# Kernel tuning notes

Measured on AMD Instinct MI355X. Metric: run time of the kernel, lower is better.

Reference implementation:

```python
import jax, jax.numpy as jnp
import numpy as np

N_HEAD = 16
N_BLOCKS = 2
EPS = 1e-6

def _rmsnorm(x, g):
    return x * jax.lax.rsqrt(jnp.mean(x * x, axis=-1, keepdims=True) + EPS) * g

def _causal_sa(x, Wqkv, Wproj, g):
    # x: (B, T, C); fused qkv, RMSNorm on q/k over full C before head split
    B, T, C = x.shape
    hd = C // N_HEAD
    q, k, v = jnp.split(x @ Wqkv, 3, axis=-1)
    q = _rmsnorm(q, g)
    k = _rmsnorm(k, g)
    def heads(t):
        return t.reshape(B, T, N_HEAD, hd).transpose(0, 2, 1, 3)
    q, k, v = heads(q), heads(k), heads(v)
    scores = jnp.einsum('bhqd,bhkd->bhqk', q, k) * (1.0 / np.sqrt(hd))
    mask = jnp.tril(jnp.ones((T, T), dtype=bool))
    scores = jnp.where(mask, scores, -jnp.finfo(scores.dtype).max)
    att = jax.nn.softmax(scores, axis=-1)
    y = jnp.einsum('bhqk,bhkd->bhqd', att, v)
    y = y.transpose(0, 2, 1, 3).reshape(B, T, C)
    return y @ Wproj

def setup_inputs() -> dict:
    key = jax.random.key(0)
    ks = jax.random.split(key, 8)
    B, ng, T, C = 2, 8, 256, 1024
    M_loc, M_glob = 16, 16
    s = 0.02
    return {
        'x': jax.random.normal(ks[0], (B, ng, T, C), jnp.float32),
        'mem_tokens': jax.random.normal(ks[1], (B, M_glob, C), jnp.float32),
        'local_mem': jax.random.normal(ks[2], (B, ng, M_loc, C), jnp.float32),
        'Wqkv_loc': jax.random.normal(ks[3], (N_BLOCKS, C, 3 * C), jnp.float32) * s,
        'Wproj_loc': jax.random.normal(ks[4], (N_BLOCKS, C, C), jnp.float32) * s,
        'g_loc': jnp.ones((N_BLOCKS, C), jnp.float32),
        'Wqkv_glob': jax.random.normal(ks[5], (N_BLOCKS, C, 3 * C), jnp.float32) * s,
        'Wproj_glob': jax.random.normal(ks[6], (N_BLOCKS, C, C), jnp.float32) * s,
        'g_glob': jnp.ones((N_BLOCKS, C), jnp.float32),
    }

def reference(x, mem_tokens, local_mem, Wqkv_loc, Wproj_loc, g_loc, Wqkv_glob, Wproj_glob, g_glob):
    B, ng, T, C = x.shape
    M_loc = local_mem.shape[2]
    M_glob = mem_tokens.shape[1]
    for i in range(N_BLOCKS):
        # local causal SA: per-group, with local mem tokens prepended
        xl = jnp.concatenate([local_mem, x], axis=2).reshape(B * ng, M_loc + T, C)
        yl = _causal_sa(xl, Wqkv_loc[i], Wproj_loc[i], g_loc[i])
        yl = yl.reshape(B, ng, M_loc + T, C)
        local_mem = yl[:, :, :M_loc, :]
        x = yl[:, :, M_loc:, :]
        # global causal SA over flattened sequence with global mem tokens
        xg = x.reshape(B, ng * T, C)
        xg = jnp.concatenate([mem_tokens, xg], axis=1)
        yg = _causal_sa(xg, Wqkv_glob[i], Wproj_glob[i], g_glob[i])
        mem_tokens = yg[:, :M_glob, :]
        x = yg[:, M_glob:, :].reshape(B, ng, T, C)
    return x
```

## Files before the change

### kernel.cpp

```cpp
#include <hip/hip_runtime.h>
#include <hip/hip_bf16.h>
#include <math.h>

typedef __attribute__((ext_vector_type(8))) short s16x8;
typedef __attribute__((ext_vector_type(4))) short s16x4;
typedef __attribute__((ext_vector_type(4))) float f32x4;

#define MPAD 4352
#define LG 2064
#define CT 8
#define SM_SHIFT 11.5415603f

__device__ __forceinline__ short f2b(float f) {
  unsigned u = __float_as_uint(f);
  unsigned r = (u + 0x7fffu + ((u >> 16) & 1u)) >> 16;
  return (short)(unsigned short)r;
}
__device__ __forceinline__ float b2f(short s) {
  return __uint_as_float(((unsigned)(unsigned short)s) << 16);
}
__device__ __forceinline__ float fexp2(float x) {
#if __has_builtin(__builtin_amdgcn_exp2f)
  return __builtin_amdgcn_exp2f(x);
#else
  float r;
  asm("v_exp_f32 %0, %1" : "=v"(r) : "v"(x));
  return r;
#endif
}
__device__ __forceinline__ int cvtpk(float lo, float hi) {
  int r;
  asm("v_cvt_pk_bf16_f32 %0, %1, %2" : "=v"(r) : "v"(lo), "v"(hi));
  return r;
}

__device__ __forceinline__ void gl_lds16(const short* g, short* l) {
  __builtin_amdgcn_global_load_lds((const __attribute__((address_space(1))) short*)g,
                                   (__attribute__((address_space(3))) short*)l, 16, 0, 0);
}

__global__ __launch_bounds__(256) void transpose_cast(const float* __restrict__ in,
                                                      short* __restrict__ out,
                                                      int K, int N) {
  __shared__ float tile[32][33];
  int bn = blockIdx.x * 32;
  int bk = blockIdx.y * 32;
  for (int i = threadIdx.y; i < 32; i += 8)
    tile[i][threadIdx.x] = in[(size_t)(bk + i) * N + bn + threadIdx.x];
  __syncthreads();
  for (int i = threadIdx.y; i < 32; i += 8)
    out[(size_t)(bn + i) * K + bk + threadIdx.x] = f2b(tile[threadIdx.x][i]);
}

__global__ __launch_bounds__(256) void transpose_v(const short* __restrict__ QKV,
                                                   short* __restrict__ Vt,
                                                   int L, int Lpad) {
  __shared__ short tile[32][33];
  int sh = blockIdx.z;
  int s = sh >> 4, h = sh & 15;
  int kb = blockIdx.x * 32;
  int cb = blockIdx.y * 32;
  int tx = threadIdx.x;
  for (int i = threadIdx.y; i < 32; i += 8) {
    int key = kb + i;
    if (key > L - 1) key = L - 1;
    tile[i][tx] = QKV[(size_t)(s * L + key) * 3072 + 2048 + h * 64 + cb + tx];
  }
  __syncthreads();
  for (int i = threadIdx.y; i < 32; i += 8)
    Vt[((size_t)sh * 64 + cb + i) * Lpad + kb + tx] = tile[tx][i];
}

#define QROW(MI, AX)                                                                  \
  acc[MI][0] = __builtin_amdgcn_mfma_f32_16x16x32_bf16(AX, b0, acc[MI][0], 0, 0, 0);  \
  acc[MI][1] = __builtin_amdgcn_mfma_f32_16x16x32_bf16(AX, b1, acc[MI][1], 0, 0, 0);  \
  acc[MI][2] = __builtin_amdgcn_mfma_f32_16x16x32_bf16(AX, b2, acc[MI][2], 0, 0, 0);  \
  acc[MI][3] = __builtin_amdgcn_mfma_f32_16x16x32_bf16(AX, b3, acc[MI][3], 0, 0, 0);

#define RD12(B, S)                                                              \
  a0 = rdA(B, S, 0); a1 = rdA(B, S, 1); a2 = rdA(B, S, 2); a3 = rdA(B, S, 3);   \
  a4 = rdA(B, S, 4); a5 = rdA(B, S, 5); a6 = rdA(B, S, 6); a7 = rdA(B, S, 7);   \
  b0 = rdB(B, S, 0); b1 = rdB(B, S, 1); b2 = rdB(B, S, 2); b3 = rdB(B, S, 3);

__global__ __launch_bounds__(512, 2) void gemm_8ph(const short* __restrict__ A,
                                                   const short* __restrict__ BT,
                                                   short* __restrict__ C,
                                                   int K, int N) {
  extern __shared__ short lds[];
  short* Asb = lds;
  short* Bsb = lds + 32768;
  const int tid = threadIdx.x;
  const int lane = tid & 63, wid = tid >> 6;
  const int wm = wid >> 2, wn = wid & 3;
  const int l15 = lane & 15, lhi = lane >> 4;
  const int m0 = blockIdx.y * 256;
  const int n0 = blockIdx.x * 256;

  f32x4 acc[8][4] = {};

  auto stageA = [&](int b, int h, int kt) {
#pragma unroll
    for (int j = 0; j < 2; ++j) {
      int u = j * 512 + tid;
      int row = u >> 3, slot = u & 7;
      int ss = slot ^ (row & 7);
      gl_lds16(A + (size_t)(m0 + h * 128 + row) * K + kt * 64 + ss * 8,
               Asb + (b * 2 + h) * 8192 + u * 8);
    }
  };
  auto stageB = [&](int b, int h, int kt) {
#pragma unroll
    for (int j = 0; j < 2; ++j) {
      int u = j * 512 + tid;
      int row = u >> 3, slot = u & 7;
      int ss = slot ^ (row & 7);
      gl_lds16(BT + (size_t)(n0 + h * 128 + row) * K + kt * 64 + ss * 8,
               Bsb + (b * 2 + h) * 8192 + u * 8);
    }
  };
  auto rdA = [&](int b, int s, int mf) -> s16x8 {
    int row = mf * 16 + l15;
    int sl = ((s << 2) | lhi) ^ (row & 7);
    return *(const s16x8*)(Asb + (b * 2 + wm) * 8192 + row * 64 + sl * 8);
  };
  auto rdB = [&](int b, int s, int nf) -> s16x8 {
    int row = (wn & 1) * 64 + nf * 16 + l15;
    int sl = ((s << 2) | lhi) ^ (row & 7);
    return *(const s16x8*)(Bsb + (b * 2 + (wn >> 1)) * 8192 + row * 64 + sl * 8);
  };

  const int NT = K >> 7;

  stageA(0, 0, 0); stageA(0, 1, 0); stageB(0, 0, 0); stageB(0, 1, 0);
  stageA(1, 0, 1); stageA(1, 1, 1);
  asm volatile("s_waitcnt vmcnt(4)" ::: "memory");
  __builtin_amdgcn_s_barrier();

  s16x8 a0, a1, a2, a3, a4, a5, a6, a7, b0, b1, b2, b3;

  for (int t = 0; t < NT; ++t) {
    const bool last = (t == NT - 1);
    const int kt1 = 2 * t + 1;
    RD12(0, 0)
    stageB(1, 0, kt1);
    __builtin_amdgcn_s_barrier();
    __builtin_amdgcn_s_setprio(1);
    QROW(0, a0) QROW(1, a1) QROW(2, a2) QROW(3, a3)
    __builtin_amdgcn_s_setprio(0);
    __builtin_amdgcn_s_barrier();
    stageB(1, 1, kt1);
    __builtin_amdgcn_s_barrier();
    __builtin_amdgcn_s_setprio(1);
    QROW(4, a4) QROW(5, a5) QROW(6, a6) QROW(7, a7)
    __builtin_amdgcn_s_setprio(0);
    __builtin_amdgcn_s_barrier();
    RD12(0, 1)
    __builtin_amdgcn_s_barrier();
    __builtin_amdgcn_s_setprio(1);
    QROW(0, a0) QROW(1, a1) QROW(2, a2) QROW(3, a3)
    __builtin_amdgcn_s_setprio(0);
    __builtin_amdgcn_s_barrier();
    if (!last) {
      stageA(0, 0, 2 * t + 2); stageA(0, 1, 2 * t + 2);
      asm volatile("s_waitcnt vmcnt(4)" ::: "memory");
    } else {
      asm volatile("s_waitcnt vmcnt(0)" ::: "memory");
    }
    __builtin_amdgcn_s_barrier();
    __builtin_amdgcn_s_setprio(1);
    QROW(4, a4) QROW(5, a5) QROW(6, a6) QROW(7, a7)
    __builtin_amdgcn_s_setprio(0);
    __builtin_amdgcn_s_barrier();
    RD12(1, 0)
    if (!last) stageB(0, 0, 2 * t + 2);
    __builtin_amdgcn_s_barrier();
    __builtin_amdgcn_s_setprio(1);
    QROW(0, a0) QROW(1, a1) QROW(2, a2) QROW(3, a3)
    __builtin_amdgcn_s_setprio(0);
    __builtin_amdgcn_s_barrier();
    if (!last) stageB(0, 1, 2 * t + 2);
    __builtin_amdgcn_s_barrier();
    __builtin_amdgcn_s_setprio(1);
    QROW(4, a4) QROW(5, a5) QROW(6, a6) QROW(7, a7)
    __builtin_amdgcn_s_setprio(0);
    __builtin_amdgcn_s_barrier();
    RD12(1, 1)
    __builtin_amdgcn_s_barrier();
    __builtin_amdgcn_s_setprio(1);
    QROW(0, a0) QROW(1, a1) QROW(2, a2) QROW(3, a3)
    __builtin_amdgcn_s_setprio(0);
    __builtin_amdgcn_s_barrier();
    if (!last) {
      stageA(1, 0, kt1 + 2); stageA(1, 1, kt1 + 2);
      asm volatile("s_waitcnt vmcnt(4)" ::: "memory");
    }
    __builtin_amdgcn_s_barrier();
    __builtin_amdgcn_s_setprio(1);
    QROW(4, a4) QROW(5, a5) QROW(6, a6) QROW(7, a7)
    __builtin_amdgcn_s_setprio(0);
    __builtin_amdgcn_s_barrier();
  }

#pragma unroll
  for (int mf = 0; mf < 8; ++mf) {
    int row_base = m0 + wm * 128 + mf * 16 + lhi * 4;
#pragma unroll
    for (int nf = 0; nf < 4; ++nf) {
      int col = n0 + wn * 64 + nf * 16 + l15;
#pragma unroll
      for (int r = 0; r < 4; ++r)
        C[(size_t)(row_base + r) * N + col] = f2b(acc[mf][nf][r]);
    }
  }
}

__global__ __launch_bounds__(256) void gemm_bt3(const short* __restrict__ A,
                                                const short* __restrict__ BT,
                                                short* __restrict__ C,
                                                int K, int N) {
  __shared__ short As[2][128 * 32];
  __shared__ short Bs[2][128 * 32];
  const int tid = threadIdx.x;
  const int lane = tid & 63;
  const int w = tid >> 6;
  const int wr = (w >> 1) * 64, wc = (w & 1) * 64;
  const int m0 = blockIdx.y * 128;
  const int n0 = blockIdx.x * 128;
  const int l15 = lane & 15, lhi = lane >> 4;

  f32x4 acc[4][4] = {};

  auto STAGE = [&](int b, int k0) {
#pragma unroll
    for (int p = 0; p < 2; ++p) {
      int g = w * 128 + p * 64 + lane;
      int row = g >> 2;
      int cs = (g & 3) * 8;
      gl_lds16(A + (size_t)(m0 + row) * K + k0 + cs, &As[b][g * 8]);
      gl_lds16(BT + (size_t)(n0 + row) * K + k0 + cs, &Bs[b][g * 8]);
    }
  };

  const int nt = K >> 5;
  STAGE(0, 0);
  __syncthreads();
  int cur = 0;
  for (int t = 0; t < nt; ++t) {
    if (t + 1 < nt) STAGE(cur ^ 1, (t + 1) << 5);
    s16x8 af[4], bf[4];
#pragma unroll
    for (int m = 0; m < 4; ++m)
      af[m] = *(const s16x8*)(&As[cur][(wr + m * 16 + l15) * 32 + lhi * 8]);
#pragma unroll
    for (int n = 0; n < 4; ++n)
      bf[n] = *(const s16x8*)(&Bs[cur][(wc + n * 16 + l15) * 32 + lhi * 8]);
#pragma unroll
    for (int m = 0; m < 4; ++m)
#pragma unroll
      for (int n = 0; n < 4; ++n)
        acc[m][n] = __builtin_amdgcn_mfma_f32_16x16x32_bf16(af[m], bf[n], acc[m][n], 0, 0, 0);
    __syncthreads();
    cur ^= 1;
  }
#pragma unroll
  for (int m = 0; m < 4; ++m) {
    int row_base = m0 + wr + m * 16 + lhi * 4;
#pragma unroll
    for (int n = 0; n < 4; ++n) {
      int col = n0 + wc + n * 16 + l15;
#pragma unroll
      for (int r = 0; r < 4; ++r)
        C[(size_t)(row_base + r) * N + col] = f2b(acc[m][n][r]);
    }
  }
}

__global__ __launch_bounds__(256) void rmsnorm_qk(short* __restrict__ QKV,
                                                  const float* __restrict__ g) {
  int row = blockIdx.x;
  int which = blockIdx.y;
  size_t base = (size_t)row * 3072 + (size_t)which * 1024;
  int t = threadIdx.x;
  s16x4 in = *(const s16x4*)(QKV + base + t * 4);
  float v[4];
  float ss = 0.f;
#pragma unroll
  for (int j = 0; j < 4; ++j) {
    v[j] = b2f(in[j]);
    ss += v[j] * v[j];
  }
#pragma unroll
  for (int m = 32; m >= 1; m >>= 1) ss += __shfl_xor(ss, m);
  __shared__ float red[4];
  if ((t & 63) == 0) red[t >> 6] = ss;
  __syncthreads();
  float tot = red[0] + red[1] + red[2] + red[3];
  float inv = rsqrtf(tot * (1.0f / 1024.0f) + 1e-6f);
  if (which == 0) inv *= 0.125f * 1.44269504f;
  s16x4 out;
#pragma unroll
  for (int j = 0; j < 4; ++j) out[j] = f2b(v[j] * inv * g[t * 4 + j]);
  *(s16x4*)(&QKV[base + t * 4]) = out;
}

__global__ __launch_bounds__(256) void attn_causal4(const short* __restrict__ QKV,
                                                    const short* __restrict__ Vt,
                                                    short* __restrict__ Y,
                                                    int L, int Lpad) {
  const int h = blockIdx.y, s = blockIdx.z;
  const int q0 = blockIdx.x * 64;
  const int tid = threadIdx.x;
  const int lane = tid & 63, w = tid >> 6;
  const int l15 = lane & 15, lhi = lane >> 4;
  const int row0 = s * L;

  __shared__ short Ks[2][64][72];
  __shared__ short Vs[2][64][72];

  int qld = q0 + w * 16 + l15;
  if (qld > L - 1) qld = L - 1;
  const size_t qrow = (size_t)(row0 + qld) * 3072 + h * 64;
  s16x8 qf0 = *(const s16x8*)(QKV + qrow + lhi * 8);
  s16x8 qf1 = *(const s16x8*)(QKV + qrow + 32 + lhi * 8);

  float lsum = 0.f;
  f32x4 o[4];
#pragma unroll
  for (int d = 0; d < 4; ++d) o[d] = f32x4{0.f, 0.f, 0.f, 0.f};

  const short* Vbase = Vt + (size_t)(s * 16 + h) * 64 * Lpad;
  const int sA = (lhi & 1) * 32 + l15;
  const int sB = sA + 16;
  const int bh = lhi >> 1;

  s16x8 kreg[2], vreg[2];
#pragma unroll
  for (int p = 0; p < 2; ++p) {
    int g = tid + p * 256;
    int kr = g >> 3, cs = (g & 7) * 8;
    int krow = kr;
    if (krow > L - 1) krow = L - 1;
    kreg[p] = *(const s16x8*)(QKV + (size_t)(row0 + krow) * 3072 + 1024 + h * 64 + cs);
    vreg[p] = *(const s16x8*)(Vbase + (size_t)kr * Lpad + cs);
  }

  int buf = 0;
  for (int kb = 0; kb <= q0; kb += 64, buf ^= 1) {
#pragma unroll
    for (int p = 0; p < 2; ++p) {
      int g = tid + p * 256;
      int kr = g >> 3, cs = (g & 7) * 8;
      *(s16x8*)(&Ks[buf][kr][cs]) = kreg[p];
      *(s16x8*)(&Vs[buf][kr][cs]) = vreg[p];
    }
    __syncthreads();
    if (kb + 64 <= q0) {
#pragma unroll
      for (int p = 0; p < 2; ++p) {
        int g = tid + p * 256;
        int kr = g >> 3, cs = (g & 7) * 8;
        int krow = kb + 64 + kr;
        if (krow > L - 1) krow = L - 1;
        kreg[p] = *(const s16x8*)(QKV + (size_t)(row0 + krow) * 3072 + 1024 + h * 64 + cs);
        vreg[p] = *(const s16x8*)(Vbase + (size_t)kr * Lpad + kb + 64 + cs);
      }
    }

    f32x4 st[4];
#pragma unroll
    for (int n = 0; n < 4; ++n) {
      s16x8 k0 = *(const s16x8*)(&Ks[buf][n * 16 + l15][lhi * 8]);
      s16x8 k1 = *(const s16x8*)(&Ks[buf][n * 16 + l15][32 + lhi * 8]);
      f32x4 sa = f32x4{-SM_SHIFT, -SM_SHIFT, -SM_SHIFT, -SM_SHIFT};
      sa = __builtin_amdgcn_mfma_f32_16x16x32_bf16(k0, qf0, sa, 0, 0, 0);
      sa = __builtin_amdgcn_mfma_f32_16x16x32_bf16(k1, qf1, sa, 0, 0, 0);
      st[n] = sa;
    }

    if (kb == q0) {
      int q = q0 + w * 16 + l15;
#pragma unroll
      for (int n = 0; n < 4; ++n) {
#pragma unroll
        for (int r = 0; r < 4; ++r) {
          int key = kb + n * 16 + lhi * 4 + r;
          if (key > q) st[n][r] = -1e30f;
        }
      }
    }

    int wd[4][2];
#pragma unroll
    for (int n = 0; n < 4; ++n) {
      float p0 = fexp2(st[n][0]), p1 = fexp2(st[n][1]);
      float p2 = fexp2(st[n][2]), p3 = fexp2(st[n][3]);
      lsum += (p0 + p1) + (p2 + p3);
      wd[n][0] = cvtpk(p0, p1);
      wd[n][1] = cvtpk(p2, p3);
    }

#pragma unroll
    for (int kk = 0; kk < 2; ++kk) {
      int a0 = __shfl(wd[2 * kk][0], sA), a1 = __shfl(wd[2 * kk][1], sA);
      int a2 = __shfl(wd[2 * kk][0], sB), a3 = __shfl(wd[2 * kk][1], sB);
      int c0 = __shfl(wd[2 * kk + 1][0], sA), c1 = __shfl(wd[2 * kk + 1][1], sA);
      int c2 = __shfl(wd[2 * kk + 1][0], sB), c3 = __shfl(wd[2 * kk + 1][1], sB);
      int pw[4];
      pw[0] = bh ? c0 : a0;
      pw[1] = bh ? c1 : a1;
      pw[2] = bh ? c2 : a2;
      pw[3] = bh ? c3 : a3;
      s16x8 pa = *(const s16x8*)pw;
#pragma unroll
      for (int d = 0; d < 4; ++d) {
        s16x8 vf = *(const s16x8*)(&Vs[buf][d * 16 + l15][kk * 32 + lhi * 8]);
        o[d] = __builtin_amdgcn_mfma_f32_16x16x32_bf16(pa, vf, o[d], 0, 0, 0);
      }
    }
  }

  lsum += __shfl_xor(lsum, 16);
  lsum += __shfl_xor(lsum, 32);
  float lsq[4];
#pragma unroll
  for (int r = 0; r < 4; ++r) lsq[r] = __shfl(lsum, lhi * 4 + r);
#pragma unroll
  for (int d = 0; d < 4; ++d) {
#pragma unroll
    for (int r = 0; r < 4; ++r) {
      int qr = q0 + w * 16 + lhi * 4 + r;
      if (qr < L)
        Y[(size_t)(row0 + qr) * 1024 + h * 64 + d * 16 + l15] = f2b(o[d][r] / lsq[r]);
    }
  }
}

__global__ __launch_bounds__(256) void attn_split2(const short* __restrict__ QKV,
                                                   const short* __restrict__ Vt,
                                                   float* __restrict__ o_acc,
                                                   float* __restrict__ ls_acc) {
  const int qb = blockIdx.x;
  const int chunk = blockIdx.y;
  const int sh = blockIdx.z;
  const int t0 = chunk * CT;
  if (t0 > qb) return;
  const int t1 = min(t0 + CT, qb + 1);
  const int h = sh & 15, s = sh >> 4;
  const int q0 = qb * 64;
  const int tid = threadIdx.x;
  const int lane = tid & 63, w = tid >> 6;
  const int l15 = lane & 15, lhi = lane >> 4;
  const int row0 = s * LG;
  const int Lpad = 2112;

  __shared__ short Ks[2][64][72];
  __shared__ short Vs[2][64][72];

  int qld = q0 + w * 16 + l15;
  if (qld > LG - 1) qld = LG - 1;
  const size_t qrow = (size_t)(row0 + qld) * 3072 + h * 64;
  s16x8 qf0 = *(const s16x8*)(QKV + qrow + lhi * 8);
  s16x8 qf1 = *(const s16x8*)(QKV + qrow + 32 + lhi * 8);

  float lsum = 0.f;
  f32x4 o[4];
#pragma unroll
  for (int d = 0; d < 4; ++d) o[d] = f32x4{0.f, 0.f, 0.f, 0.f};

  const short* Vbase = Vt + (size_t)sh * 64 * Lpad;
  const int sA = (lhi & 1) * 32 + l15;
  const int sB = sA + 16;
  const int bh = lhi >> 1;

  s16x8 kreg[2], vreg[2];
  const int kb0 = t0 * 64;
#pragma unroll
  for (int p = 0; p < 2; ++p) {
    int g = tid + p * 256;
    int kr = g >> 3, cs = (g & 7) * 8;
    int krow = kb0 + kr;
    if (krow > LG - 1) krow = LG - 1;
    kreg[p] = *(const s16x8*)(QKV + (size_t)(row0 + krow) * 3072 + 1024 + h * 64 + cs);
    vreg[p] = *(const s16x8*)(Vbase + (size_t)kr * Lpad + kb0 + cs);
  }

  int buf = 0;
  for (int t = t0; t < t1; ++t, buf ^= 1) {
    const int kb = t * 64;
#pragma unroll
    for (int p = 0; p < 2; ++p) {
      int g = tid + p * 256;
      int kr = g >> 3, cs = (g & 7) * 8;
      *(s16x8*)(&Ks[buf][kr][cs]) = kreg[p];
      *(s16x8*)(&Vs[buf][kr][cs]) = vreg[p];
    }
    __syncthreads();
    if (t + 1 < t1) {
#pragma unroll
      for (int p = 0; p < 2; ++p) {
        int g = tid + p * 256;
        int kr = g >> 3, cs = (g & 7) * 8;
        int krow = kb + 64 + kr;
        if (krow > LG - 1) krow = LG - 1;
        kreg[p] = *(const s16x8*)(QKV + (size_t)(row0 + krow) * 3072 + 1024 + h * 64 + cs);
        vreg[p] = *(const s16x8*)(Vbase + (size_t)kr * Lpad + kb + 64 + cs);
      }
    }

    f32x4 st[4];
#pragma unroll
    for (int n = 0; n < 4; ++n) {
      s16x8 k0 = *(const s16x8*)(&Ks[buf][n * 16 + l15][lhi * 8]);
      s16x8 k1 = *(const s16x8*)(&Ks[buf][n * 16 + l15][32 + lhi * 8]);
      f32x4 sa = f32x4{-SM_SHIFT, -SM_SHIFT, -SM_SHIFT, -SM_SHIFT};
      sa = __builtin_amdgcn_mfma_f32_16x16x32_bf16(k0, qf0, sa, 0, 0, 0);
      sa = __builtin_amdgcn_mfma_f32_16x16x32_bf16(k1, qf1, sa, 0, 0, 0);
      st[n] = sa;
    }

    if (t == qb) {
      int q = q0 + w * 16 + l15;
#pragma unroll
      for (int n = 0; n < 4; ++n) {
#pragma unroll
        for (int r = 0; r < 4; ++r) {
          int key = kb + n * 16 + lhi * 4 + r;
          if (key > q) st[n][r] = -1e30f;
        }
      }
    }

    int wd[4][2];
#pragma unroll
    for (int n = 0; n < 4; ++n) {
      float p0 = fexp2(st[n][0]), p1 = fexp2(st[n][1]);
      float p2 = fexp2(st[n][2]), p3 = fexp2(st[n][3]);
      lsum += (p0 + p1) + (p2 + p3);
      wd[n][0] = cvtpk(p0, p1);
      wd[n][1] = cvtpk(p2, p3);
    }

#pragma unroll
    for (int kk = 0; kk < 2; ++kk) {
      int a0 = __shfl(wd[2 * kk][0], sA), a1 = __shfl(wd[2 * kk][1], sA);
      int a2 = __shfl(wd[2 * kk][0], sB), a3 = __shfl(wd[2 * kk][1], sB);
      int c0 = __shfl(wd[2 * kk + 1][0], sA), c1 = __shfl(wd[2 * kk + 1][1], sA);
      int c2 = __shfl(wd[2 * kk + 1][0], sB), c3 = __shfl(wd[2 * kk + 1][1], sB);
      int pw[4];
      pw[0] = bh ? c0 : a0;
      pw[1] = bh ? c1 : a1;
      pw[2] = bh ? c2 : a2;
      pw[3] = bh ? c3 : a3;
      s16x8 pa = *(const s16x8*)pw;
#pragma unroll
      for (int d = 0; d < 4; ++d) {
        s16x8 vf = *(const s16x8*)(&Vs[buf][d * 16 + l15][kk * 32 + lhi * 8]);
        o[d] = __builtin_amdgcn_mfma_f32_16x16x32_bf16(pa, vf, o[d], 0, 0, 0);
      }
    }
  }

  lsum += __shfl_xor(lsum, 16);
  lsum += __shfl_xor(lsum, 32);
  int qmy = q0 + w * 16 + l15;
  if (lhi == 0 && qmy < LG) atomicAdd(&ls_acc[(size_t)sh * LG + qmy], lsum);
#pragma unroll
  for (int r = 0; r < 4; ++r) {
    int qr = q0 + w * 16 + lhi * 4 + r;
    if (qr < LG) {
#pragma unroll
      for (int d = 0; d < 4; ++d)
        atomicAdd(&o_acc[((size_t)sh * LG + qr) * 64 + d * 16 + l15], o[d][r]);
    }
  }
}

__global__ __launch_bounds__(256) void attn_merge(const float* __restrict__ o_acc,
                                                  const float* __restrict__ ls_acc,
                                                  short* __restrict__ Y) {
  int sh = blockIdx.z * 16 + blockIdx.y;
  int s = sh >> 4, h = sh & 15;
  int row = blockIdx.x * 4 + (threadIdx.x >> 6);
  int col = threadIdx.x & 63;
  if (row < LG) {
    float inv = 1.0f / ls_acc[(size_t)sh * LG + row];
    float v = o_acc[((size_t)sh * LG + row) * 64 + col];
    Y[(size_t)(s * LG + row) * 1024 + h * 64 + col] = f2b(v * inv);
  }
}

__global__ __launch_bounds__(256) void build_xl(const float* __restrict__ x,
                                                const float* __restrict__ lm,
                                                short* __restrict__ Xin) {
  int row = blockIdx.x;
  int s = row / 272, r = row % 272;
  const float* src = (r < 16) ? lm + ((size_t)s * 16 + r) * 1024
                              : x + ((size_t)s * 256 + (r - 16)) * 1024;
  int t = threadIdx.x;
  f32x4 v = *(const f32x4*)(src + t * 4);
  s16x4 o;
#pragma unroll
  for (int j = 0; j < 4; ++j) o[j] = f2b(v[j]);
  *(s16x4*)(&Xin[(size_t)row * 1024 + t * 4]) = o;
}

__global__ __launch_bounds__(256) void split_local_build_xg(const short* __restrict__ Pout,
                                                            const float* __restrict__ mem_src,
                                                            float* __restrict__ lm_out,
                                                            short* __restrict__ Xin) {
  int row = blockIdx.x;
  int t = threadIdx.x;
  if (row < 4352) {
    int sr = row < 4128 ? row : 4127;
    int b = sr / 2064, r = sr % 2064;
    s16x4 o;
    if (r < 16) {
      f32x4 v = *(const f32x4*)(mem_src + ((size_t)(b * 16 + r)) * 1024 + t * 4);
#pragma unroll
      for (int j = 0; j < 4; ++j) o[j] = f2b(v[j]);
    } else {
      int f = b * 2048 + (r - 16);
      int pr = (f >> 8) * 272 + 16 + (f & 255);
      o = *(const s16x4*)(Pout + (size_t)pr * 1024 + t * 4);
    }
    *(s16x4*)(&Xin[(size_t)row * 1024 + t * 4]) = o;
  } else {
    int m = row - 4352;
    int pr = (m >> 4) * 272 + (m & 15);
    s16x4 v = *(const s16x4*)(Pout + (size_t)pr * 1024 + t * 4);
    f32x4 o;
#pragma unroll
    for (int j = 0; j < 4; ++j) o[j] = b2f(v[j]);
    *(f32x4*)(&lm_out[(size_t)m * 1024 + t * 4]) = o;
  }
}

__global__ __launch_bounds__(256) void split_global_build_xl(const short* __restrict__ Pout,
                                                             const float* __restrict__ lm_src,
                                                             float* __restrict__ mem_out,
                                                             short* __restrict__ Xin) {
  int row = blockIdx.x;
  int t = threadIdx.x;
  if (row < 4352) {
    int s = row / 272, r = row % 272;
    s16x4 o;
    if (r < 16) {
      f32x4 v = *(const f32x4*)(lm_src + ((size_t)(s * 16 + r)) * 1024 + t * 4);
#pragma unroll
      for (int j = 0; j < 4; ++j) o[j] = f2b(v[j]);
    } else {
      int f = s * 256 + (r - 16);
      int pr = (f >> 11) * 2064 + 16 + (f & 2047);
      o = *(const s16x4*)(Pout + (size_t)pr * 1024 + t * 4);
    }
    *(s16x4*)(&Xin[(size_t)row * 1024 + t * 4]) = o;
  } else {
    int m = row - 4352;
    int pr = (m >> 4) * 2064 + (m & 15);
    s16x4 v = *(const s16x4*)(Pout + (size_t)pr * 1024 + t * 4);
    f32x4 o;
#pragma unroll
    for (int j = 0; j < 4; ++j) o[j] = b2f(v[j]);
    *(f32x4*)(&mem_out[(size_t)m * 1024 + t * 4]) = o;
  }
}

__global__ __launch_bounds__(256) void split_global_final(const short* __restrict__ Pout,
                                                          float* __restrict__ out) {
  int f = blockIdx.x;
  int t = threadIdx.x;
  int pr = (f >> 11) * 2064 + 16 + (f & 2047);
  s16x4 v = *(const s16x4*)(Pout + (size_t)pr * 1024 + t * 4);
  f32x4 o;
#pragma unroll
  for (int j = 0; j < 4; ++j) o[j] = b2f(v[j]);
  *(f32x4*)(&out[(size_t)f * 1024 + t * 4]) = o;
}

extern "C" void kernel_launch(void* const* d_in, const int* in_sizes, int n_in,
                              void* d_out, int out_size, void* d_ws, size_t ws_size,
                              hipStream_t stream) {
  const float* x_in = (const float*)d_in[0];
  const float* mem_in = (const float*)d_in[1];
  const float* lm_in = (const float*)d_in[2];
  const float* Wqkv_loc = (const float*)d_in[3];
  const float* Wproj_loc = (const float*)d_in[4];
  const float* g_loc = (const float*)d_in[5];
  const float* Wqkv_glob = (const float*)d_in[6];
  const float* Wproj_glob = (const float*)d_in[7];
  const float* g_glob = (const float*)d_in[8];

  static bool attr_set = false;
  if (!attr_set) {
    hipFuncSetAttribute((const void*)gemm_8ph,
                        hipFuncAttributeMaxDynamicSharedMemorySize, 131072);
    attr_set = true;
  }

  char* ws = (char*)d_ws;
  size_t off = 0;
  auto alloc = [&](size_t bytes) {
    char* p = ws + off;
    off += (bytes + 255) & ~(size_t)255;
    return p;
  };
  short* Wt = (short*)alloc((size_t)3072 * 1024 * 2);
  float* lm_cur = (float*)alloc((size_t)256 * 1024 * 4);
  float* mem_cur = (float*)alloc((size_t)32 * 1024 * 4);
  short* Xin = (short*)alloc((size_t)MPAD * 1024 * 2);
  short* QKVb = (short*)alloc((size_t)MPAD * 3072 * 2);
  short* Yb = (short*)alloc((size_t)MPAD * 1024 * 2);
  short* Pout = (short*)alloc((size_t)MPAD * 1024 * 2);
  short* Vtb = (short*)alloc((size_t)256 * 64 * 320 * 2);
  size_t oacc_bytes = (size_t)32 * LG * 64 * 4;
  size_t lacc_bytes = (size_t)32 * LG * 4;
  float* o_acc = (float*)alloc(oacc_bytes);
  float* ls_acc = (float*)alloc(lacc_bytes);
  const bool use_split = (ws_size >= off);

  for (int i = 0; i < 2; ++i) {
    transpose_cast<<<dim3(96, 32), dim3(32, 8), 0, stream>>>(
        Wqkv_loc + (size_t)i * 1024 * 3072, Wt, 1024, 3072);
    if (i == 0) build_xl<<<4352, 256, 0, stream>>>(x_in, lm_in, Xin);
    gemm_8ph<<<dim3(12, 17), 512, 131072, stream>>>(Xin, Wt, QKVb, 1024, 3072);
    rmsnorm_qk<<<dim3(4352, 2), 256, 0, stream>>>(QKVb, g_loc + (size_t)i * 1024);
    transpose_v<<<dim3(10, 2, 256), dim3(32, 8), 0, stream>>>(QKVb, Vtb, 272, 320);
    attn_causal4<<<dim3(5, 16, 16), 256, 0, stream>>>(QKVb, Vtb, Yb, 272, 320);
    transpose_cast<<<dim3(32, 32), dim3(32, 8), 0, stream>>>(
        Wproj_loc + (size_t)i * 1024 * 1024, Wt, 1024, 1024);
    gemm_bt3<<<dim3(8, 34), 256, 0, stream>>>(Yb, Wt, Pout, 1024, 1024);
    split_local_build_xg<<<4608, 256, 0, stream>>>(Pout, i == 0 ? mem_in : mem_cur,
                                                   lm_cur, Xin);

    transpose_cast<<<dim3(96, 32), dim3(32, 8), 0, stream>>>(
        Wqkv_glob + (size_t)i * 1024 * 3072, Wt, 1024, 3072);
    gemm_8ph<<<dim3(12, 17), 512, 131072, stream>>>(Xin, Wt, QKVb, 1024, 3072);
    rmsnorm_qk<<<dim3(4128, 2), 256, 0, stream>>>(QKVb, g_glob + (size_t)i * 1024);
    transpose_v<<<dim3(66, 2, 32), dim3(32, 8), 0, stream>>>(QKVb, Vtb, 2064, 2112);
    if (use_split) {
      hipMemsetAsync(o_acc, 0, oacc_bytes, stream);
      hipMemsetAsync(ls_acc, 0, lacc_bytes, stream);
      attn_split2<<<dim3(33, 5, 32), 256, 0, stream>>>(QKVb, Vtb, o_acc, ls_acc);
      attn_merge<<<dim3(516, 16, 2), 256, 0, stream>>>(o_acc, ls_acc, Yb);
    } else {
      attn_causal4<<<dim3(33, 16, 2), 256, 0, stream>>>(QKVb, Vtb, Yb, 2064, 2112);
    }
    transpose_cast<<<dim3(32, 32), dim3(32, 8), 0, stream>>>(
        Wproj_glob + (size_t)i * 1024 * 1024, Wt, 1024, 1024);
    gemm_bt3<<<dim3(8, 34), 256, 0, stream>>>(Yb, Wt, Pout, 1024, 1024);
    if (i == 0)
      split_global_build_xl<<<4384, 256, 0, stream>>>(Pout, lm_cur, mem_cur, Xin);
    else
      split_global_final<<<4096, 256, 0, stream>>>(Pout, (float*)d_out);
  }
}
```

Before: 529.6 us.

## Load K/V MFMA fragments directly from global memory, dropping LDS staging

Both attention kernels (causal and split-K global) no longer stage K and V tiles through double-buffered shared memory with block barriers. Each wave now loads its MFMA operand fragments for K and the transposed V straight from global memory into registers every key block. This removes LDS writes and reads and the __syncthreads per iteration. In exchange, each of the four waves reloads the same K/V data, relying on L1/L2 to absorb it, and the explicit prefetch overlap of the next tile is lost.

```diff
diff --git a/kernel.cpp b/kernel.cpp
--- a/kernel.cpp
+++ b/kernel.cpp
@@ -303,7 +303,8 @@
   *(s16x4*)(&QKV[base + t * 4]) = out;
 }
 
-__global__ __launch_bounds__(256) void attn_causal4(const short* __restrict__ QKV,
+
+__global__ __launch_bounds__(256) void attn_causal5(const short* __restrict__ QKV,
                                                     const short* __restrict__ Vt,
                                                     short* __restrict__ Y,
                                                     int L, int Lpad) {
@@ -314,9 +315,6 @@
   const int l15 = lane & 15, lhi = lane >> 4;
   const int row0 = s * L;
 
-  __shared__ short Ks[2][64][72];
-  __shared__ short Vs[2][64][72];
-
   int qld = q0 + w * 16 + l15;
   if (qld > L - 1) qld = L - 1;
   const size_t qrow = (size_t)(row0 + qld) * 3072 + h * 64;
@@ -333,47 +331,28 @@
   const int sB = sA + 16;
   const int bh = lhi >> 1;
 
-  s16x8 kreg[2], vreg[2];
-#pragma unroll
-  for (int p = 0; p < 2; ++p) {
-    int g = tid + p * 256;
-    int kr = g >> 3, cs = (g & 7) * 8;
-    int krow = kr;
-    if (krow > L - 1) krow = L - 1;
-    kreg[p] = *(const s16x8*)(QKV + (size_t)(row0 + krow) * 3072 + 1024 + h * 64 + cs);
-    vreg[p] = *(const s16x8*)(Vbase + (size_t)kr * Lpad + cs);
-  }
-
-  int buf = 0;
-  for (int kb = 0; kb <= q0; kb += 64, buf ^= 1) {
-#pragma unroll
-    for (int p = 0; p < 2; ++p) {
-      int g = tid + p * 256;
-      int kr = g >> 3, cs = (g & 7) * 8;
-      *(s16x8*)(&Ks[buf][kr][cs]) = kreg[p];
-      *(s16x8*)(&Vs[buf][kr][cs]) = vreg[p];
-    }
-    __syncthreads();
-    if (kb + 64 <= q0) {
-#pragma unroll
-      for (int p = 0; p < 2; ++p) {
-        int g = tid + p * 256;
-        int kr = g >> 3, cs = (g & 7) * 8;
-        int krow = kb + 64 + kr;
-        if (krow > L - 1) krow = L - 1;
-        kreg[p] = *(const s16x8*)(QKV + (size_t)(row0 + krow) * 3072 + 1024 + h * 64 + cs);
-        vreg[p] = *(const s16x8*)(Vbase + (size_t)kr * Lpad + kb + 64 + cs);
-      }
-    }
+  for (int kb = 0; kb <= q0; kb += 64) {
+    s16x8 kf0[4], kf1[4], vfr[2][4];
+#pragma unroll
+    for (int n = 0; n < 4; ++n) {
+      int krow = kb + n * 16 + l15;
+      if (krow > L - 1) krow = L - 1;
+      const short* kp = QKV + (size_t)(row0 + krow) * 3072 + 1024 + h * 64;
+      kf0[n] = *(const s16x8*)(kp + lhi * 8);
+      kf1[n] = *(const s16x8*)(kp + 32 + lhi * 8);
+    }
+#pragma unroll
+    for (int kk = 0; kk < 2; ++kk)
+#pragma unroll
+      for (int d = 0; d < 4; ++d)
+        vfr[kk][d] = *(const s16x8*)(Vbase + (size_t)(d * 16 + l15) * Lpad + kb + kk * 32 + lhi * 8);
 
     f32x4 st[4];
 #pragma unroll
     for (int n = 0; n < 4; ++n) {
-      s16x8 k0 = *(const s16x8*)(&Ks[buf][n * 16 + l15][lhi * 8]);
-      s16x8 k1 = *(const s16x8*)(&Ks[buf][n * 16 + l15][32 + lhi * 8]);
       f32x4 sa = f32x4{-SM_SHIFT, -SM_SHIFT, -SM_SHIFT, -SM_SHIFT};
-      sa = __builtin_amdgcn_mfma_f32_16x16x32_bf16(k0, qf0, sa, 0, 0, 0);
-      sa = __builtin_amdgcn_mfma_f32_16x16x32_bf16(k1, qf1, sa, 0, 0, 0);
+      sa = __builtin_amdgcn_mfma_f32_16x16x32_bf16(kf0[n], qf0, sa, 0, 0, 0);
+      sa = __builtin_amdgcn_mfma_f32_16x16x32_bf16(kf1[n], qf1, sa, 0, 0, 0);
       st[n] = sa;
     }
 
@@ -412,10 +391,8 @@
       pw[3] = bh ? c3 : a3;
       s16x8 pa = *(const s16x8*)pw;
 #pragma unroll
-      for (int d = 0; d < 4; ++d) {
-        s16x8 vf = *(const s16x8*)(&Vs[buf][d * 16 + l15][kk * 32 + lhi * 8]);
-        o[d] = __builtin_amdgcn_mfma_f32_16x16x32_bf16(pa, vf, o[d], 0, 0, 0);
-      }
+      for (int d = 0; d < 4; ++d)
+        o[d] = __builtin_amdgcn_mfma_f32_16x16x32_bf16(pa, vfr[kk][d], o[d], 0, 0, 0);
     }
   }
 
@@ -435,7 +412,7 @@
   }
 }
 
-__global__ __launch_bounds__(256) void attn_split2(const short* __restrict__ QKV,
+__global__ __launch_bounds__(256) void attn_split3(const short* __restrict__ QKV,
                                                    const short* __restrict__ Vt,
                                                    float* __restrict__ o_acc,
                                                    float* __restrict__ ls_acc) {
@@ -453,9 +430,6 @@
   const int row0 = s * LG;
   const int Lpad = 2112;
 
-  __shared__ short Ks[2][64][72];
-  __shared__ short Vs[2][64][72];
-
   int qld = q0 + w * 16 + l15;
   if (qld > LG - 1) qld = LG - 1;
   const size_t qrow = (size_t)(row0 + qld) * 3072 + h * 64;
@@ -472,49 +446,29 @@
   const int sB = sA + 16;
   const int bh = lhi >> 1;
 
-  s16x8 kreg[2], vreg[2];
-  const int kb0 = t0 * 64;
-#pragma unroll
-  for (int p = 0; p < 2; ++p) {
-    int g = tid + p * 256;
-    int kr = g >> 3, cs = (g & 7) * 8;
-    int krow = kb0 + kr;
-    if (krow > LG - 1) krow = LG - 1;
-    kreg[p] = *(const s16x8*)(QKV + (size_t)(row0 + krow) * 3072 + 1024 + h * 64 + cs);
-    vreg[p] = *(const s16x8*)(Vbase + (size_t)kr * Lpad + kb0 + cs);
-  }
-
-  int buf = 0;
-  for (int t = t0; t < t1; ++t, buf ^= 1) {
+  for (int t = t0; t < t1; ++t) {
     const int kb = t * 64;
-#pragma unroll
-    for (int p = 0; p < 2; ++p) {
-      int g = tid + p * 256;
-      int kr = g >> 3, cs = (g & 7) * 8;
-      *(s16x8*)(&Ks[buf][kr][cs]) = kreg[p];
-      *(s16x8*)(&Vs[buf][kr][cs]) = vreg[p];
-    }
-    __syncthreads();
-    if (t + 1 < t1) {
-#pragma unroll
-      for (int p = 0; p < 2; ++p) {
-        int g = tid + p * 256;
-        int kr = g >> 3, cs = (g & 7) * 8;
-        int krow = kb + 64 + kr;
-        if (krow > LG - 1) krow = LG - 1;
-        kreg[p] = *(const s16x8*)(QKV + (size_t)(row0 + krow) * 3072 + 1024 + h * 64 + cs);
-        vreg[p] = *(const s16x8*)(Vbase + (size_t)kr * Lpad + kb + 64 + cs);
-      }
-    }
+    s16x8 kf0[4], kf1[4], vfr[2][4];
+#pragma unroll
+    for (int n = 0; n < 4; ++n) {
+      int krow = kb + n * 16 + l15;
+      if (krow > LG - 1) krow = LG - 1;
+      const short* kp = QKV + (size_t)(row0 + krow) * 3072 + 1024 + h * 64;
+      kf0[n] = *(const s16x8*)(kp + lhi * 8);
+      kf1[n] = *(const s16x8*)(kp + 32 + lhi * 8);
+    }
+#pragma unroll
+    for (int kk = 0; kk < 2; ++kk)
+#pragma unroll
+      for (int d = 0; d < 4; ++d)
+        vfr[kk][d] = *(const s16x8*)(Vbase + (size_t)(d * 16 + l15) * Lpad + kb + kk * 32 + lhi * 8);
 
     f32x4 st[4];
 #pragma unroll
     for (int n = 0; n < 4; ++n) {
-      s16x8 k0 = *(const s16x8*)(&Ks[buf][n * 16 + l15][lhi * 8]);
-      s16x8 k1 = *(const s16x8*)(&Ks[buf][n * 16 + l15][32 + lhi * 8]);
       f32x4 sa = f32x4{-SM_SHIFT, -SM_SHIFT, -SM_SHIFT, -SM_SHIFT};
-      sa = __builtin_amdgcn_mfma_f32_16x16x32_bf16(k0, qf0, sa, 0, 0, 0);
-      sa = __builtin_amdgcn_mfma_f32_16x16x32_bf16(k1, qf1, sa, 0, 0, 0);
+      sa = __builtin_amdgcn_mfma_f32_16x16x32_bf16(kf0[n], qf0, sa, 0, 0, 0);
+      sa = __builtin_amdgcn_mfma_f32_16x16x32_bf16(kf1[n], qf1, sa, 0, 0, 0);
       st[n] = sa;
     }
 
@@ -553,10 +507,8 @@
       pw[3] = bh ? c3 : a3;
       s16x8 pa = *(const s16x8*)pw;
 #pragma unroll
-      for (int d = 0; d < 4; ++d) {
-        s16x8 vf = *(const s16x8*)(&Vs[buf][d * 16 + l15][kk * 32 + lhi * 8]);
-        o[d] = __builtin_amdgcn_mfma_f32_16x16x32_bf16(pa, vf, o[d], 0, 0, 0);
-      }
+      for (int d = 0; d < 4; ++d)
+        o[d] = __builtin_amdgcn_mfma_f32_16x16x32_bf16(pa, vfr[kk][d], o[d], 0, 0, 0);
     }
   }
 
@@ -725,7 +677,7 @@
     gemm_8ph<<<dim3(12, 17), 512, 131072, stream>>>(Xin, Wt, QKVb, 1024, 3072);
     rmsnorm_qk<<<dim3(4352, 2), 256, 0, stream>>>(QKVb, g_loc + (size_t)i * 1024);
     transpose_v<<<dim3(10, 2, 256), dim3(32, 8), 0, stream>>>(QKVb, Vtb, 272, 320);
-    attn_causal4<<<dim3(5, 16, 16), 256, 0, stream>>>(QKVb, Vtb, Yb, 272, 320);
+    attn_causal5<<<dim3(5, 16, 16), 256, 0, stream>>>(QKVb, Vtb, Yb, 272, 320);
     transpose_cast<<<dim3(32, 32), dim3(32, 8), 0, stream>>>(
         Wproj_loc + (size_t)i * 1024 * 1024, Wt, 1024, 1024);
     gemm_bt3<<<dim3(8, 34), 256, 0, stream>>>(Yb, Wt, Pout, 1024, 1024);
@@ -740,10 +692,10 @@
     if (use_split) {
       hipMemsetAsync(o_acc, 0, oacc_bytes, stream);
       hipMemsetAsync(ls_acc, 0, lacc_bytes, stream);
-      attn_split2<<<dim3(33, 5, 32), 256, 0, stream>>>(QKVb, Vtb, o_acc, ls_acc);
+      attn_split3<<<dim3(33, 5, 32), 256, 0, stream>>>(QKVb, Vtb, o_acc, ls_acc);
       attn_merge<<<dim3(516, 16, 2), 256, 0, stream>>>(o_acc, ls_acc, Yb);
     } else {
-      attn_causal4<<<dim3(33, 16, 2), 256, 0, stream>>>(QKVb, Vtb, Yb, 2064, 2112);
+      attn_causal5<<<dim3(33, 16, 2), 256, 0, stream>>>(QKVb, Vtb, Yb, 2064, 2112);
     }
     transpose_cast<<<dim3(32, 32), dim3(32, 8), 0, stream>>>(
         Wproj_glob + (size_t)i * 1024 * 1024, Wt, 1024, 1024);
```

Measured after the change: 767.7 us. +45.0%, slower.
